# Performance work log

Measured on AMD Instinct MI355X. Metric: run time of the kernel, lower is better.

## Reference

```python
import jax, jax.numpy as jnp
import numpy as np

NUM_HEADS = 12
TOP_P = 0.9


def setup_inputs() -> dict:
    key = jax.random.key(0)
    ks = jax.random.split(key, 5)
    B, N, C = 2, 2048, 768
    return {
        "x": jax.random.normal(ks[0], (B, N, C), jnp.float32),
        "qkv_w": jax.random.normal(ks[1], (3 * C, C), jnp.float32) * (C ** -0.5),
        "proj_w": jax.random.normal(ks[2], (C, C), jnp.float32) * (C ** -0.5),
        "proj_b": jax.random.normal(ks[3], (C,), jnp.float32) * 0.02,
        "temperature": jnp.ones((1,), jnp.float32),
        "top_k": 64,
    }


def reference(x, qkv_w, proj_w, proj_b, temperature, top_k):
    B, N, C = x.shape
    H = NUM_HEADS
    D = C // H
    # qkv projection: [B,N,3C] -> [3,B,H,N,D]
    qkv = (x @ qkv_w.T).reshape(B, N, 3, H, D).transpose(2, 0, 3, 1, 4)
    q, k, v = qkv[0], qkv[1], qkv[2]
    scale = (D ** -0.5) * temperature  # (1,) broadcasts
    attn = jnp.einsum("bhnd,bhmd->bhnm", q, k) * scale  # [B,H,N,N]
    neg_inf = jnp.asarray(-jnp.inf, attn.dtype)
    # top-k filtering: keep only scores >= k-th largest per row
    kth = jax.lax.top_k(attn, top_k)[0][..., -1:]
    attn = jnp.where(attn < kth, neg_inf, attn)
    # top-p (nucleus) filtering on sorted scores
    order = jnp.argsort(-attn, axis=-1)  # descending sort indices
    sorted_attn = jnp.take_along_axis(attn, order, axis=-1)
    cum = jnp.cumsum(jax.nn.softmax(sorted_attn, axis=-1), axis=-1)
    rm = cum > TOP_P
    # shift right by one, always keep the top entry
    rm = jnp.concatenate([jnp.zeros_like(rm[..., :1]), rm[..., :-1]], axis=-1)
    # scatter back to original positions via inverse permutation
    inv = jnp.argsort(order, axis=-1)
    remove = jnp.take_along_axis(rm, inv, axis=-1)
    attn = jnp.where(remove, neg_inf, attn)
    p = jax.nn.softmax(attn, axis=-1)
    out = jnp.einsum("bhnm,bhmd->bhnd", p, v)  # [B,H,N,D]
    out = out.transpose(0, 2, 1, 3).reshape(B, N, C)
    return out @ proj_w.T + proj_b
```

## Files before the change

### kernel.cpp

```cpp
#include <hip/hip_runtime.h>
#include <cstdint>

#define NH 12
#define HD 64
#define NSEQ 2048
#define CDIM 768
#define NB 2

typedef __attribute__((ext_vector_type(2))) float f32x2;

__global__ __launch_bounds__(256, 4) void qkv_qk(const float* __restrict__ x,
                                                 const float* __restrict__ w,
                                                 double* __restrict__ Q64,
                                                 double* __restrict__ K64,
                                                 float* __restrict__ Qs32,
                                                 float* __restrict__ Kt32) {
    __shared__ double As[16][128];
    __shared__ double Bs[16][64];
    const int tid = threadIdx.x;
    const int bm = blockIdx.y * 128;
    const int bn = blockIdx.x * 64;
    const int alm = tid >> 1, alk = (tid & 1) * 8;
    const int blm = tid & 63, blk = (tid >> 6) * 4;
    const int tx = tid & 15, ty = tid >> 4;

    double acc[8][4] = {};
    float4 a0 = *reinterpret_cast<const float4*>(&x[(bm + alm) * CDIM + alk]);
    float4 a1 = *reinterpret_cast<const float4*>(&x[(bm + alm) * CDIM + alk + 4]);
    float4 b0 = *reinterpret_cast<const float4*>(&w[(bn + blm) * CDIM + blk]);
    for (int k0 = 0; k0 < CDIM; k0 += 16) {
        __syncthreads();
        As[alk + 0][alm] = (double)a0.x; As[alk + 1][alm] = (double)a0.y;
        As[alk + 2][alm] = (double)a0.z; As[alk + 3][alm] = (double)a0.w;
        As[alk + 4][alm] = (double)a1.x; As[alk + 5][alm] = (double)a1.y;
        As[alk + 6][alm] = (double)a1.z; As[alk + 7][alm] = (double)a1.w;
        Bs[blk + 0][blm] = (double)b0.x; Bs[blk + 1][blm] = (double)b0.y;
        Bs[blk + 2][blm] = (double)b0.z; Bs[blk + 3][blm] = (double)b0.w;
        __syncthreads();
        if (k0 + 16 < CDIM) {
            a0 = *reinterpret_cast<const float4*>(&x[(bm + alm) * CDIM + k0 + 16 + alk]);
            a1 = *reinterpret_cast<const float4*>(&x[(bm + alm) * CDIM + k0 + 16 + alk + 4]);
            b0 = *reinterpret_cast<const float4*>(&w[(bn + blm) * CDIM + k0 + 16 + blk]);
        }
#pragma unroll
        for (int k = 0; k < 16; ++k) {
            double ad[8], bd[4];
#pragma unroll
            for (int i = 0; i < 8; ++i) ad[i] = As[k][ty * 8 + i];
#pragma unroll
            for (int j = 0; j < 4; ++j) bd[j] = Bs[k][tx * 4 + j];
#pragma unroll
            for (int i = 0; i < 8; ++i)
#pragma unroll
                for (int j = 0; j < 4; ++j) acc[i][j] = fma(ad[i], bd[j], acc[i][j]);
        }
    }
    const bool isQ = bn < CDIM;
    const int hh = (isQ ? bn : bn - CDIM) >> 6;
    const int b  = bm >> 11;
    const int bh = b * NH + hh;
#pragma unroll
    for (int i = 0; i < 8; ++i) {
        const int n = (bm + ty * 8 + i) & (NSEQ - 1);
        const size_t base = ((size_t)bh * NSEQ + n) * HD + tx * 4;
        if (isQ) {
            double2 d01; d01.x = acc[i][0]; d01.y = acc[i][1];
            double2 d23; d23.x = acc[i][2]; d23.y = acc[i][3];
            *reinterpret_cast<double2*>(&Q64[base]) = d01;
            *reinterpret_cast<double2*>(&Q64[base + 2]) = d23;
            *reinterpret_cast<float4*>(&Qs32[base]) =
                make_float4((float)acc[i][0], (float)acc[i][1], (float)acc[i][2], (float)acc[i][3]);
        } else {
            double2 d01; d01.x = acc[i][0]; d01.y = acc[i][1];
            double2 d23; d23.x = acc[i][2]; d23.y = acc[i][3];
            *reinterpret_cast<double2*>(&K64[base]) = d01;
            *reinterpret_cast<double2*>(&K64[base + 2]) = d23;
#pragma unroll
            for (int j = 0; j < 4; ++j)
                Kt32[((size_t)bh * HD + tx * 4 + j) * NSEQ + n] = (float)acc[i][j];
        }
    }
}

__global__ __launch_bounds__(256) void qkv_v(const float* __restrict__ x,
                                             const float* __restrict__ wv,
                                             float* __restrict__ V) {
    __shared__ float As[16][64];
    __shared__ float Bs[16][64];
    const int tid = threadIdx.x;
    const int bm = blockIdx.y * 64;
    const int bn = blockIdx.x * 64;
    const int lm = tid >> 2;
    const int lk = (tid & 3) << 2;
    const int tx = tid & 15, ty = tid >> 4;

    float acc[4][4] = {};
    float4 av = *reinterpret_cast<const float4*>(&x[(bm + lm) * CDIM + lk]);
    float4 bv = *reinterpret_cast<const float4*>(&wv[(bn + lm) * CDIM + lk]);
    for (int k0 = 0; k0 < CDIM; k0 += 16) {
        __syncthreads();
        As[lk + 0][lm] = av.x; As[lk + 1][lm] = av.y; As[lk + 2][lm] = av.z; As[lk + 3][lm] = av.w;
        Bs[lk + 0][lm] = bv.x; Bs[lk + 1][lm] = bv.y; Bs[lk + 2][lm] = bv.z; Bs[lk + 3][lm] = bv.w;
        __syncthreads();
        if (k0 + 16 < CDIM) {
            av = *reinterpret_cast<const float4*>(&x[(bm + lm) * CDIM + k0 + 16 + lk]);
            bv = *reinterpret_cast<const float4*>(&wv[(bn + lm) * CDIM + k0 + 16 + lk]);
        }
#pragma unroll
        for (int k = 0; k < 16; ++k) {
            float4 a4 = *reinterpret_cast<const float4*>(&As[k][ty * 4]);
            float4 b4 = *reinterpret_cast<const float4*>(&Bs[k][tx * 4]);
            float aa[4] = {a4.x, a4.y, a4.z, a4.w};
            float bb[4] = {b4.x, b4.y, b4.z, b4.w};
#pragma unroll
            for (int i = 0; i < 4; ++i)
#pragma unroll
                for (int j = 0; j < 4; ++j) acc[i][j] = fmaf(aa[i], bb[j], acc[i][j]);
        }
    }
    const int hh = bn >> 6;
    const int b  = bm >> 11;
#pragma unroll
    for (int i = 0; i < 4; ++i) {
        const int n = (bm + ty * 4 + i) & (NSEQ - 1);
        *reinterpret_cast<float4*>(&V[(((size_t)b * NH + hh) * NSEQ + n) * HD + tx * 4]) =
            make_float4(acc[i][0], acc[i][1], acc[i][2], acc[i][3]);
    }
}

__device__ inline unsigned long long d2key(double f) {
    unsigned long long u = (unsigned long long)__double_as_longlong(f);
    return u ^ (unsigned long long)(((long long)u >> 63) | (long long)0x8000000000000000ull);
}
__device__ inline double key2d(unsigned long long k) {
    unsigned long long mask = ((long long)k < 0) ? 0x8000000000000000ull : 0xFFFFFFFFFFFFFFFFull;
    return __longlong_as_double((long long)(k ^ mask));
}
__device__ inline unsigned kp(float a, float b) {
    unsigned ua = __float_as_uint(a);
    ua ^= (unsigned)(((int)ua >> 31) | 0x80000000);
    unsigned ub = __float_as_uint(b);
    ub ^= (unsigned)(((int)ub >> 31) | 0x80000000);
    return (ua >> 16) | (ub & 0xFFFF0000u);
}

__global__ __launch_bounds__(512, 6) void attn_kernel(const double* __restrict__ Q64,
                                                      const double* __restrict__ K64,
                                                      const float* __restrict__ Qs32,
                                                      const float* __restrict__ Kt32,
                                                      const float* __restrict__ V,
                                                      const float* __restrict__ temp,
                                                      const int* __restrict__ topk_p,
                                                      float* __restrict__ AO) {
    __shared__ unsigned short sk[8][NSEQ];
    __shared__ int cand[8][128];

    const int tid  = threadIdx.x;
    const int wg   = (blockIdx.x & 7) * 768 + (blockIdx.x >> 3);
    const int bh   = wg >> 8;
    const int g0   = (wg & 255) << 3;
    const int lane = tid & 63;
    const int wv   = tid >> 6;

    const double scale = 0.125 * (double)temp[0];
    const float sc32 = (float)scale;
    int TK = *topk_p;
    if (TK > 64) TK = 64;
    if (TK < 1)  TK = 1;

    const float* __restrict__ kb = Kt32 + (size_t)bh * HD * NSEQ;
    const float* __restrict__ qp = Qs32 + ((size_t)bh * NSEQ + g0) * HD;
    const int m0 = tid * 4;
    f32x2 acc2[8][2] = {};
#pragma unroll 4
    for (int d = 0; d < HD; ++d) {
        float4 k4 = *reinterpret_cast<const float4*>(&kb[(size_t)d * NSEQ + m0]);
        f32x2 kA; kA.x = k4.x; kA.y = k4.y;
        f32x2 kB; kB.x = k4.z; kB.y = k4.w;
#pragma unroll
        for (int r8 = 0; r8 < 8; ++r8) {
            float qv = qp[r8 * HD + d];
            f32x2 qq; qq.x = qv; qq.y = qv;
            acc2[r8][0] = __builtin_elementwise_fma(qq, kA, acc2[r8][0]);
            acc2[r8][1] = __builtin_elementwise_fma(qq, kB, acc2[r8][1]);
        }
    }
#pragma unroll
    for (int r8 = 0; r8 < 8; ++r8) {
        uint2 pkv;
        pkv.x = kp(acc2[r8][0].x * sc32, acc2[r8][0].y * sc32);
        pkv.y = kp(acc2[r8][1].x * sc32, acc2[r8][1].y * sc32);
        *reinterpret_cast<uint2*>(&sk[r8][m0]) = pkv;
    }
    __syncthreads();

    const int r = wv;
    const int row = g0 + r;

    int k32[32];
#pragma unroll
    for (int i = 0; i < 32; ++i) k32[i] = sk[r][i * 64 + lane];

    int mx = k32[0];
#pragma unroll
    for (int i = 1; i < 32; ++i) mx = max(mx, k32[i]);
#pragma unroll
    for (int off = 32; off > 0; off >>= 1) mx = max(mx, __shfl_xor(mx, off));

    int lo0 = mx > 1024 ? mx - 1024 : 0;
    int c0 = 0;
#pragma unroll
    for (int i = 0; i < 32; ++i) c0 += (int)__popcll(__ballot(k32[i] >= lo0));
    int lo, hi, clo;
    if (c0 >= TK) { lo = lo0; clo = c0; hi = mx; }
    else          { lo = 0;   clo = NSEQ; hi = lo0 - 1; }
    while (lo < hi && clo > 72) {
        int mid = lo + ((hi - lo + 1) >> 1);
        int c = 0;
#pragma unroll
        for (int i = 0; i < 32; ++i) c += (int)__popcll(__ballot(k32[i] >= mid));
        if (c >= TK) { lo = mid; clo = c; } else hi = mid - 1;
    }
    int thr = lo >= 2 ? lo - 2 : 0;

    const unsigned long long lmask = (1ull << lane) - 1ull;
    int base = 0;
#pragma unroll
    for (int i = 0; i < 32; ++i) {
        bool pred = k32[i] >= thr;
        unsigned long long bal = __ballot(pred);
        if (pred) {
            int slot = base + (int)__popcll(bal & lmask);
            if (slot < 128) cand[r][slot] = i * 64 + lane;
        }
        base += (int)__popcll(bal);
    }
    int ncand = min(base, 128);
    asm volatile("s_waitcnt lgkmcnt(0)" ::: "memory");

    const int gidx = lane >> 3;
    const int sl   = lane & 7;
    const double* __restrict__ qrow = Q64 + ((size_t)bh * NSEQ + row) * HD;
    double qd[8];
#pragma unroll
    for (int j = 0; j < 8; ++j) qd[j] = qrow[sl * 8 + j];

    int msArr[16];
#pragma unroll
    for (int j = 0; j < 16; ++j) msArr[j] = cand[r][min(j * 8 + gidx, ncand - 1)];

    unsigned long long* pkr = reinterpret_cast<unsigned long long*>(&sk[r][0]);
    pkr[lane] = 0ull;
    pkr[64 + lane] = 0ull;
    const double* __restrict__ kbase = K64 + (size_t)bh * NSEQ * HD;
    const int jmax = (ncand + 7) >> 3;
#pragma unroll 2
    for (int j = 0; j < jmax; ++j) {
        const int s = j * 8 + gidx;
        const int ms = msArr[j];
        const double* __restrict__ kp8 = kbase + (size_t)ms * HD + sl * 8;
        double a = 0.0;
#pragma unroll
        for (int d = 0; d < 8; ++d) a = fma(qd[d], kp8[d], a);
        a += __shfl_xor(a, 1);
        a += __shfl_xor(a, 2);
        a += __shfl_xor(a, 4);
        a *= scale;
        unsigned long long pkv = (d2key(a) & ~2047ull) | (unsigned long long)(2047 - ms);
        if (sl == (j & 7) && s < ncand) pkr[s] = pkv;
    }
    asm volatile("s_waitcnt lgkmcnt(0)" ::: "memory");
    unsigned long long pk1 = pkr[lane];
    unsigned long long pk2 = pkr[64 + lane];

    unsigned long long t0 = ~pk1, t1 = ~pk2;
#pragma unroll
    for (int k = 2; k <= 64; k <<= 1) {
#pragma unroll
        for (int j = k >> 1; j > 0; j >>= 1) {
            {
                unsigned long long ot = __shfl_xor(t0, j);
                bool dir = (lane & k) != 0;
                bool lower = (lane & j) == 0;
                bool takeMin = (lower != dir);
                bool less = t0 < ot;
                t0 = (takeMin == less) ? t0 : ot;
            }
            {
                unsigned long long ot = __shfl_xor(t1, j);
                bool dir = (k == 64) ? true : ((lane & k) != 0);
                bool lower = (lane & j) == 0;
                bool takeMin = (lower != dir);
                bool less = t1 < ot;
                t1 = (takeMin == less) ? t1 : ot;
            }
        }
    }
    {
        unsigned long long na = (t1 < t0) ? t1 : t0;
        unsigned long long nb = (t1 < t0) ? t0 : t1;
        t0 = na; t1 = nb;
    }
#pragma unroll
    for (int j = 32; j > 0; j >>= 1) {
        {
            unsigned long long ot = __shfl_xor(t0, j);
            bool lower = (lane & j) == 0;
            bool less = t0 < ot;
            t0 = (lower == less) ? t0 : ot;
        }
        {
            unsigned long long ot = __shfl_xor(t1, j);
            bool lower = (lane & j) == 0;
            bool less = t1 < ot;
            t1 = (lower == less) ? t1 : ot;
        }
    }
    unsigned long long kk = ~t0;
    int mi = 2047 - (int)(kk & 2047ull);
    bool valid = lane < TK;
    double a = valid ? key2d(kk & ~2047ull) : 0.0;
    double amax = __shfl(a, 0);
    double s = valid ? exp(a - amax) : 0.0;

    double ps = s;
#pragma unroll
    for (int off = 1; off < 64; off <<= 1) {
        double tt = __shfl_up(ps, off);
        if (lane >= off) ps += tt;
    }
    double S = __shfl(ps, 63);
    double cumprev = (ps - s) / S;
    bool keep = valid && ((lane == 0) || (cumprev <= 0.9));
    double sk2 = keep ? s : 0.0;
    double S2 = sk2;
#pragma unroll
    for (int off = 32; off > 0; off >>= 1) S2 += __shfl_xor(S2, off);
    float p = (float)(keep ? (s / S2) : 0.0);

    unsigned long long bal = __ballot(keep);
    int nk = __popcll(bal);

    const float* __restrict__ vb = V + (size_t)bh * NSEQ * HD;
    float o = 0.f;
    for (int i = 0; i < nk; ++i) {
        float pi = __shfl(p, i);
        int midx = __shfl(mi, i);
        o = fmaf(pi, vb[(size_t)midx * HD + lane], o);
    }
    const int b = bh / NH, hh = bh % NH;
    AO[((size_t)b * NSEQ + row) * CDIM + hh * HD + lane] = o;
}

__global__ __launch_bounds__(256) void proj_gemm(const float* __restrict__ A,
                                                 const float* __restrict__ w,
                                                 const float* __restrict__ bias,
                                                 float* __restrict__ out) {
    __shared__ float As[16][128];
    __shared__ float Bs[16][64];
    const int tid = threadIdx.x;
    const int bm = blockIdx.y * 128;
    const int bn = blockIdx.x * 64;
    const int alm = tid >> 1, alk = (tid & 1) * 8;
    const int blm = tid & 63, blk = (tid >> 6) * 4;
    const int tx = tid & 15, ty = tid >> 4;

    float acc[8][4] = {};
    float4 a0 = *reinterpret_cast<const float4*>(&A[(bm + alm) * CDIM + alk]);
    float4 a1 = *reinterpret_cast<const float4*>(&A[(bm + alm) * CDIM + alk + 4]);
    float4 b0 = *reinterpret_cast<const float4*>(&w[(bn + blm) * CDIM + blk]);
    for (int k0 = 0; k0 < CDIM; k0 += 16) {
        __syncthreads();
        As[alk + 0][alm] = a0.x; As[alk + 1][alm] = a0.y;
        As[alk + 2][alm] = a0.z; As[alk + 3][alm] = a0.w;
        As[alk + 4][alm] = a1.x; As[alk + 5][alm] = a1.y;
        As[alk + 6][alm] = a1.z; As[alk + 7][alm] = a1.w;
        Bs[blk + 0][blm] = b0.x; Bs[blk + 1][blm] = b0.y;
        Bs[blk + 2][blm] = b0.z; Bs[blk + 3][blm] = b0.w;
        __syncthreads();
        if (k0 + 16 < CDIM) {
            a0 = *reinterpret_cast<const float4*>(&A[(bm + alm) * CDIM + k0 + 16 + alk]);
            a1 = *reinterpret_cast<const float4*>(&A[(bm + alm) * CDIM + k0 + 16 + alk + 4]);
            b0 = *reinterpret_cast<const float4*>(&w[(bn + blm) * CDIM + k0 + 16 + blk]);
        }
#pragma unroll
        for (int k = 0; k < 16; ++k) {
            float4 af0 = *reinterpret_cast<const float4*>(&As[k][ty * 8]);
            float4 af1 = *reinterpret_cast<const float4*>(&As[k][ty * 8 + 4]);
            float4 bf  = *reinterpret_cast<const float4*>(&Bs[k][tx * 4]);
            float aa[8] = {af0.x, af0.y, af0.z, af0.w, af1.x, af1.y, af1.z, af1.w};
            float bb[4] = {bf.x, bf.y, bf.z, bf.w};
#pragma unroll
            for (int i = 0; i < 8; ++i)
#pragma unroll
                for (int j = 0; j < 4; ++j) acc[i][j] = fmaf(aa[i], bb[j], acc[i][j]);
        }
    }
    float4 bv = *reinterpret_cast<const float4*>(&bias[bn + tx * 4]);
#pragma unroll
    for (int i = 0; i < 8; ++i) {
        int rr = bm + ty * 8 + i;
        float4 v4 = make_float4(acc[i][0] + bv.x, acc[i][1] + bv.y,
                                acc[i][2] + bv.z, acc[i][3] + bv.w);
        *reinterpret_cast<float4*>(&out[(size_t)rr * CDIM + bn + tx * 4]) = v4;
    }
}

extern "C" void kernel_launch(void* const* d_in, const int* in_sizes, int n_in,
                              void* d_out, int out_size, void* d_ws, size_t ws_size,
                              hipStream_t stream) {
    const float* x      = (const float*)d_in[0];
    const float* qkv_w  = (const float*)d_in[1];
    const float* proj_w = (const float*)d_in[2];
    const float* proj_b = (const float*)d_in[3];
    const float* temp   = (const float*)d_in[4];
    const int*   topk   = (const int*)d_in[5];
    float* out = (float*)d_out;

    const size_t HSZ = (size_t)NB * NH * NSEQ * HD;
    double* Q64  = (double*)d_ws;
    double* K64  = Q64 + HSZ;
    float*  Qs32 = (float*)(K64 + HSZ);
    float*  Kt32 = Qs32 + HSZ;
    float*  V    = Kt32 + HSZ;
    float*  AO   = V + HSZ;

    qkv_qk<<<dim3(24, 32), 256, 0, stream>>>(x, qkv_w, Q64, K64, Qs32, Kt32);
    qkv_v<<<dim3(12, 64), 256, 0, stream>>>(x, qkv_w + (size_t)2 * CDIM * CDIM, V);
    attn_kernel<<<dim3(NB * NH * (NSEQ / 8)), 512, 0, stream>>>(Q64, K64, Qs32, Kt32, V, temp, topk, AO);
    proj_gemm<<<dim3(12, 32), 256, 0, stream>>>(AO, proj_w, proj_b, out);
}
```

Baseline: 715.5 us.

## Compute approximate QK scores with split-bf16 MFMA and 16 rows per block

Replaces the fp32 FMA computation of approximate attention scores with bf16 MFMA instructions, using a hi/lo split of Q and K (three products) so the result stays close to fp32. The qkv kernel now writes Q and K as hi/lo bf16 pairs in row layout instead of fp32 Q and transposed fp32 K. The attention block grows to 1024 threads handling 16 query rows, with a padded shared score buffer. The goal is to cut the ALU cost of the coarse scoring pass. The trade-off is more shared memory per block, lower occupancy, and scores that are slightly less accurate, which could shift which candidates the top-k prefilter selects.

```diff
diff --git a/kernel.cpp b/kernel.cpp
--- a/kernel.cpp
+++ b/kernel.cpp
@@ -6,15 +6,19 @@
 #define NSEQ 2048
 #define CDIM 768
 #define NB 2
-
-typedef __attribute__((ext_vector_type(2))) float f32x2;
+#define SKP 2052
+
+typedef __attribute__((ext_vector_type(8))) __bf16 bf16x8;
+typedef __attribute__((ext_vector_type(4))) float f32x4;
 
 __global__ __launch_bounds__(256, 4) void qkv_qk(const float* __restrict__ x,
                                                  const float* __restrict__ w,
                                                  double* __restrict__ Q64,
                                                  double* __restrict__ K64,
-                                                 float* __restrict__ Qs32,
-                                                 float* __restrict__ Kt32) {
+                                                 __bf16* __restrict__ Qh,
+                                                 __bf16* __restrict__ Ql,
+                                                 __bf16* __restrict__ Kh,
+                                                 __bf16* __restrict__ Kl) {
     __shared__ double As[16][128];
     __shared__ double Bs[16][64];
     const int tid = threadIdx.x;
@@ -44,11 +48,14 @@
         }
 #pragma unroll
         for (int k = 0; k < 16; ++k) {
-            double ad[8], bd[4];
-#pragma unroll
-            for (int i = 0; i < 8; ++i) ad[i] = As[k][ty * 8 + i];
-#pragma unroll
-            for (int j = 0; j < 4; ++j) bd[j] = Bs[k][tx * 4 + j];
+            double2 a01 = *reinterpret_cast<const double2*>(&As[k][ty * 8 + 0]);
+            double2 a23 = *reinterpret_cast<const double2*>(&As[k][ty * 8 + 2]);
+            double2 a45 = *reinterpret_cast<const double2*>(&As[k][ty * 8 + 4]);
+            double2 a67 = *reinterpret_cast<const double2*>(&As[k][ty * 8 + 6]);
+            double2 b01 = *reinterpret_cast<const double2*>(&Bs[k][tx * 4 + 0]);
+            double2 b23 = *reinterpret_cast<const double2*>(&Bs[k][tx * 4 + 2]);
+            double ad[8] = {a01.x, a01.y, a23.x, a23.y, a45.x, a45.y, a67.x, a67.y};
+            double bd[4] = {b01.x, b01.y, b23.x, b23.y};
 #pragma unroll
             for (int i = 0; i < 8; ++i)
 #pragma unroll
@@ -63,21 +70,28 @@
     for (int i = 0; i < 8; ++i) {
         const int n = (bm + ty * 8 + i) & (NSEQ - 1);
         const size_t base = ((size_t)bh * NSEQ + n) * HD + tx * 4;
+        double2 d01; d01.x = acc[i][0]; d01.y = acc[i][1];
+        double2 d23; d23.x = acc[i][2]; d23.y = acc[i][3];
         if (isQ) {
-            double2 d01; d01.x = acc[i][0]; d01.y = acc[i][1];
-            double2 d23; d23.x = acc[i][2]; d23.y = acc[i][3];
             *reinterpret_cast<double2*>(&Q64[base]) = d01;
             *reinterpret_cast<double2*>(&Q64[base + 2]) = d23;
-            *reinterpret_cast<float4*>(&Qs32[base]) =
-                make_float4((float)acc[i][0], (float)acc[i][1], (float)acc[i][2], (float)acc[i][3]);
+#pragma unroll
+            for (int j = 0; j < 4; ++j) {
+                float v = (float)acc[i][j];
+                __bf16 h = (__bf16)v;
+                __bf16 l = (__bf16)(v - (float)h);
+                Qh[base + j] = h; Ql[base + j] = l;
+            }
         } else {
-            double2 d01; d01.x = acc[i][0]; d01.y = acc[i][1];
-            double2 d23; d23.x = acc[i][2]; d23.y = acc[i][3];
             *reinterpret_cast<double2*>(&K64[base]) = d01;
             *reinterpret_cast<double2*>(&K64[base + 2]) = d23;
 #pragma unroll
-            for (int j = 0; j < 4; ++j)
-                Kt32[((size_t)bh * HD + tx * 4 + j) * NSEQ + n] = (float)acc[i][j];
+            for (int j = 0; j < 4; ++j) {
+                float v = (float)acc[i][j];
+                __bf16 h = (__bf16)v;
+                __bf16 l = (__bf16)(v - (float)h);
+                Kh[base + j] = h; Kl[base + j] = l;
+            }
         }
     }
 }
@@ -136,29 +150,29 @@
     unsigned long long mask = ((long long)k < 0) ? 0x8000000000000000ull : 0xFFFFFFFFFFFFFFFFull;
     return __longlong_as_double((long long)(k ^ mask));
 }
-__device__ inline unsigned kp(float a, float b) {
-    unsigned ua = __float_as_uint(a);
-    ua ^= (unsigned)(((int)ua >> 31) | 0x80000000);
-    unsigned ub = __float_as_uint(b);
-    ub ^= (unsigned)(((int)ub >> 31) | 0x80000000);
-    return (ua >> 16) | (ub & 0xFFFF0000u);
-}
-
-__global__ __launch_bounds__(512, 6) void attn_kernel(const double* __restrict__ Q64,
-                                                      const double* __restrict__ K64,
-                                                      const float* __restrict__ Qs32,
-                                                      const float* __restrict__ Kt32,
-                                                      const float* __restrict__ V,
-                                                      const float* __restrict__ temp,
-                                                      const int* __restrict__ topk_p,
-                                                      float* __restrict__ AO) {
-    __shared__ unsigned short sk[8][NSEQ];
-    __shared__ int cand[8][128];
+__device__ inline unsigned short kp1(float a) {
+    unsigned u = __float_as_uint(a);
+    u ^= (unsigned)(((int)u >> 31) | 0x80000000);
+    return (unsigned short)(u >> 16);
+}
+
+__global__ __launch_bounds__(1024, 8) void attn_kernel(const double* __restrict__ Q64,
+                                                       const double* __restrict__ K64,
+                                                       const __bf16* __restrict__ Qh,
+                                                       const __bf16* __restrict__ Ql,
+                                                       const __bf16* __restrict__ Kh,
+                                                       const __bf16* __restrict__ Kl,
+                                                       const float* __restrict__ V,
+                                                       const float* __restrict__ temp,
+                                                       const int* __restrict__ topk_p,
+                                                       float* __restrict__ AO) {
+    __shared__ unsigned short sk[16][SKP];
+    __shared__ int cand[16][128];
 
     const int tid  = threadIdx.x;
-    const int wg   = (blockIdx.x & 7) * 768 + (blockIdx.x >> 3);
-    const int bh   = wg >> 8;
-    const int g0   = (wg & 255) << 3;
+    const int wg   = (blockIdx.x & 7) * 384 + (blockIdx.x >> 3);
+    const int bh   = wg >> 7;
+    const int g0   = (wg & 127) << 4;
     const int lane = tid & 63;
     const int wv   = tid >> 6;
 
@@ -168,29 +182,35 @@
     if (TK > 64) TK = 64;
     if (TK < 1)  TK = 1;
 
-    const float* __restrict__ kb = Kt32 + (size_t)bh * HD * NSEQ;
-    const float* __restrict__ qp = Qs32 + ((size_t)bh * NSEQ + g0) * HD;
-    const int m0 = tid * 4;
-    f32x2 acc2[8][2] = {};
-#pragma unroll 4
-    for (int d = 0; d < HD; ++d) {
-        float4 k4 = *reinterpret_cast<const float4*>(&kb[(size_t)d * NSEQ + m0]);
-        f32x2 kA; kA.x = k4.x; kA.y = k4.y;
-        f32x2 kB; kB.x = k4.z; kB.y = k4.w;
-#pragma unroll
-        for (int r8 = 0; r8 < 8; ++r8) {
-            float qv = qp[r8 * HD + d];
-            f32x2 qq; qq.x = qv; qq.y = qv;
-            acc2[r8][0] = __builtin_elementwise_fma(qq, kA, acc2[r8][0]);
-            acc2[r8][1] = __builtin_elementwise_fma(qq, kB, acc2[r8][1]);
-        }
-    }
-#pragma unroll
-    for (int r8 = 0; r8 < 8; ++r8) {
-        uint2 pkv;
-        pkv.x = kp(acc2[r8][0].x * sc32, acc2[r8][0].y * sc32);
-        pkv.y = kp(acc2[r8][1].x * sc32, acc2[r8][1].y * sc32);
-        *reinterpret_cast<uint2*>(&sk[r8][m0]) = pkv;
+    {
+        const int arow = lane & 15;
+        const int aslot = (lane >> 4) * 8;
+        const size_t qoff = ((size_t)bh * NSEQ + g0 + arow) * HD + aslot;
+        bf16x8 ah0 = *reinterpret_cast<const bf16x8*>(Qh + qoff);
+        bf16x8 ah1 = *reinterpret_cast<const bf16x8*>(Qh + qoff + 32);
+        bf16x8 al0 = *reinterpret_cast<const bf16x8*>(Ql + qoff);
+        bf16x8 al1 = *reinterpret_cast<const bf16x8*>(Ql + qoff + 32);
+        const int mbase = wv * 128;
+        const int ccol = lane & 15, crow4 = (lane >> 4) * 4;
+#pragma unroll
+        for (int t = 0; t < 8; ++t) {
+            const int m0t = mbase + t * 16;
+            const size_t koff = ((size_t)bh * NSEQ + m0t + arow) * HD + aslot;
+            bf16x8 kh0 = *reinterpret_cast<const bf16x8*>(Kh + koff);
+            bf16x8 kh1 = *reinterpret_cast<const bf16x8*>(Kh + koff + 32);
+            bf16x8 kl0 = *reinterpret_cast<const bf16x8*>(Kl + koff);
+            bf16x8 kl1 = *reinterpret_cast<const bf16x8*>(Kl + koff + 32);
+            f32x4 acc = {0.f, 0.f, 0.f, 0.f};
+            acc = __builtin_amdgcn_mfma_f32_16x16x32_bf16(ah0, kh0, acc, 0, 0, 0);
+            acc = __builtin_amdgcn_mfma_f32_16x16x32_bf16(ah0, kl0, acc, 0, 0, 0);
+            acc = __builtin_amdgcn_mfma_f32_16x16x32_bf16(al0, kh0, acc, 0, 0, 0);
+            acc = __builtin_amdgcn_mfma_f32_16x16x32_bf16(ah1, kh1, acc, 0, 0, 0);
+            acc = __builtin_amdgcn_mfma_f32_16x16x32_bf16(ah1, kl1, acc, 0, 0, 0);
+            acc = __builtin_amdgcn_mfma_f32_16x16x32_bf16(al1, kh1, acc, 0, 0, 0);
+#pragma unroll
+            for (int i = 0; i < 4; ++i)
+                sk[crow4 + i][m0t + ccol] = kp1(acc[i] * sc32);
+        }
     }
     __syncthreads();
 
@@ -418,15 +438,17 @@
     float* out = (float*)d_out;
 
     const size_t HSZ = (size_t)NB * NH * NSEQ * HD;
-    double* Q64  = (double*)d_ws;
-    double* K64  = Q64 + HSZ;
-    float*  Qs32 = (float*)(K64 + HSZ);
-    float*  Kt32 = Qs32 + HSZ;
-    float*  V    = Kt32 + HSZ;
-    float*  AO   = V + HSZ;
-
-    qkv_qk<<<dim3(24, 32), 256, 0, stream>>>(x, qkv_w, Q64, K64, Qs32, Kt32);
+    double* Q64 = (double*)d_ws;
+    double* K64 = Q64 + HSZ;
+    __bf16* Qh  = (__bf16*)(K64 + HSZ);
+    __bf16* Ql  = Qh + HSZ;
+    __bf16* Kh  = Ql + HSZ;
+    __bf16* Kl  = Kh + HSZ;
+    float*  V   = (float*)(Kl + HSZ);
+    float*  AO  = V + HSZ;
+
+    qkv_qk<<<dim3(24, 32), 256, 0, stream>>>(x, qkv_w, Q64, K64, Qh, Ql, Kh, Kl);
     qkv_v<<<dim3(12, 64), 256, 0, stream>>>(x, qkv_w + (size_t)2 * CDIM * CDIM, V);
-    attn_kernel<<<dim3(NB * NH * (NSEQ / 8)), 512, 0, stream>>>(Q64, K64, Qs32, Kt32, V, temp, topk, AO);
+    attn_kernel<<<dim3(NB * NH * (NSEQ / 16)), 1024, 0, stream>>>(Q64, K64, Qh, Ql, Kh, Kl, V, temp, topk, AO);
     proj_gemm<<<dim3(12, 32), 256, 0, stream>>>(AO, proj_w, proj_b, out);
 }
```

Result: slower. 828.0 us (+15.7%).
